# Kernel optimization log

Hardware: AMD Instinct MI355X
Metric: run time of the kernel (lower is better)

Reference implementation:

```python
import jax, jax.numpy as jnp
import numpy as np
from jax import lax

C = 32    # feats_channels
CT = 16   # transform_channels
B, D, H, W = 1, 16, 16, 32  # N = D*H*W = 8192


def _bcast(v):
    return v[None, :, None, None, None]


def conv1(x, w):
    # 1x1x1 Conv3d, no bias: w [O, I], x [b, I, d, h, w]
    return jnp.einsum('oi,bidhw->bodhw', w, x)


def cbr(x, w, s, b):
    # Conv1x1x1 + inference BatchNorm (folded to scale s / bias b) + ReLU
    return jax.nn.relu(conv1(x, w) * _bcast(s) + _bcast(b))


def setup_inputs() -> dict:
    key = jax.random.key(0)
    ks = jax.random.split(key, 16)

    def wmat(k, shape, scale=0.05):
        return jax.random.normal(k, shape, jnp.float32) * scale

    def bn(k, n):
        k1, k2 = jax.random.split(k)
        s = 1.0 + 0.05 * jax.random.normal(k1, (n,), jnp.float32)
        b = 0.05 * jax.random.normal(k2, (n,), jnp.float32)
        return s, b

    inp = {'x': jax.random.normal(ks[0], (B, C, D, H, W), jnp.float32)}
    # query_project: 2 convs (C->CT, CT->CT), each conv+BN+ReLU
    inp['wq1'] = wmat(ks[1], (CT, C));  inp['sq1'], inp['bq1'] = bn(ks[2], CT)
    inp['wq2'] = wmat(ks[3], (CT, CT)); inp['sq2'], inp['bq2'] = bn(ks[4], CT)
    # key_project: 2 convs (2C->CT, CT->CT)
    inp['wk1'] = wmat(ks[5], (CT, 2 * C)); inp['sk1'], inp['bk1'] = bn(ks[6], CT)
    inp['wk2'] = wmat(ks[7], (CT, CT));    inp['sk2'], inp['bk2'] = bn(ks[8], CT)
    # value_project: 1 conv (2C->CT) + BN + ReLU
    inp['wv'] = wmat(ks[9], (CT, 2 * C)); inp['sv'], inp['bv'] = bn(ks[10], CT)
    # out_project: 1 conv (CT->C) + BN + ReLU
    inp['wo'] = wmat(ks[11], (C, CT)); inp['so'], inp['bo'] = bn(ks[12], C)
    # bottleneck: Conv3d(2C->C, k=3, pad=1, no bias) + BN + LeakyReLU(0.1)
    inp['wbot'] = wmat(ks[13], (C, 2 * C, 3, 3, 3), 0.02)
    inp['sbot'], inp['bbot'] = bn(ks[14], C)
    return inp


def reference(x, wq1, sq1, bq1, wq2, sq2, bq2,
              wk1, sk1, bk1, wk2, sk2, bk2,
              wv, sv, bv, wo, so, bo, wbot, sbot, bbot):
    b, c, d, h, w = x.shape
    # AdaptiveAvgPool2d((1,1)) on (b, c*d, h, w) = mean over (h, w) per (c,d);
    # bilinear upsample from 1x1 is a constant broadcast.
    xg = jnp.mean(x, axis=(3, 4), keepdims=True)
    key_feats = jnp.concatenate([jnp.broadcast_to(xg, x.shape), x], axis=1)  # [b, 2c, d, h, w]

    q = cbr(cbr(x, wq1, sq1, bq1), wq2, sq2, bq2)          # [b, CT, d, h, w]
    k = cbr(cbr(key_feats, wk1, sk1, bk1), wk2, sk2, bk2)  # [b, CT, d, h, w]
    v = cbr(key_feats, wv, sv, bv)                          # [b, CT, d, h, w]

    n = d * h * w
    q = q.reshape(b, CT, n).transpose(0, 2, 1)  # [b, N, CT]
    k = k.reshape(b, CT, n)                     # [b, CT, N]
    v = v.reshape(b, CT, n).transpose(0, 2, 1)  # [b, N, CT]

    sim = jnp.einsum('bnc,bcm->bnm', q, k) * (CT ** -0.5)   # [b, N, N]
    sim = jax.nn.softmax(sim, axis=-1)
    ctx = jnp.einsum('bnm,bmc->bnc', sim, v)                # [b, N, CT]
    ctx = ctx.transpose(0, 2, 1).reshape(b, CT, d, h, w)
    ctx = cbr(ctx, wo, so, bo)                              # [b, C, d, h, w]

    fused = jnp.concatenate([x, ctx], axis=1)               # [b, 2C, d, h, w]
    y = lax.conv_general_dilated(
        fused, wbot, window_strides=(1, 1, 1), padding='SAME',
        dimension_numbers=('NCDHW', 'OIDHW', 'NCDHW'))
    y = y * _bcast(sbot) + _bcast(bbot)
    return jnp.where(y > 0, y, 0.1 * y)  # LeakyReLU(0.1)
```

## Files before the change

### kernel.cpp

```cpp
#include <hip/hip_runtime.h>

typedef unsigned int u32;
typedef unsigned short u16;
typedef float f32x16 __attribute__((ext_vector_type(16)));
typedef __bf16 bf16x8 __attribute__((ext_vector_type(8)));
union BF8 { u32 w[4]; bf16x8 v; };

#define DEVI static __device__ __forceinline__
DEVI u32 pk_bf16(float lo, float hi) {
  u32 r;
  asm("v_cvt_pk_bf16_f32 %0, %1, %2" : "=v"(r) : "v"(lo), "v"(hi));
  return r;
}
DEVI u16 bf1(float x) { return (u16)(pk_bf16(x, 0.0f) & 0xffffu); }

#define WB_WREP  0
#define WB_QS    131072
#define WB_K     393216
#define WB_VT    655360
#define WB_FUS   917504

__global__ __launch_bounds__(256) void k_prep(
    const float* __restrict__ x,
    const float* __restrict__ wq1, const float* __restrict__ sq1, const float* __restrict__ bq1,
    const float* __restrict__ wq2, const float* __restrict__ sq2, const float* __restrict__ bq2,
    const float* __restrict__ wk1, const float* __restrict__ sk1, const float* __restrict__ bk1,
    const float* __restrict__ wk2, const float* __restrict__ sk2, const float* __restrict__ bk2,
    const float* __restrict__ wv,  const float* __restrict__ sv,  const float* __restrict__ bv,
    const float* __restrict__ wbot, const float* __restrict__ sbot,
    u16* __restrict__ qs, u16* __restrict__ kbm, u16* __restrict__ vt,
    u16* __restrict__ fus, u16* __restrict__ wrep) {
  const int tid = threadIdx.x;
  const int bid = blockIdx.x;
  if (bid >= 256) {
    const int rb = bid - 256;
#pragma unroll
    for (int e = 0; e < 8; ++e) {
      const int idx = rb * 2048 + tid * 8 + e;
      const int tap = idx >> 11, rem = idx & 2047, o = rem >> 6, i = rem & 63;
      wrep[idx] = bf1(wbot[(o * 64 + i) * 27 + tap] * sbot[o]);
    }
    return;
  }
  __shared__ float H[2][32][17];
  __shared__ float P8[32][8];
  __shared__ float xgs[32];
  const int n0 = bid << 5;
  const int d = n0 >> 9;
  {
    const int c = tid >> 3, part = tid & 7;
    const float4* xp = (const float4*)(x + (c << 13) + (d << 9));
    float s = 0.f;
#pragma unroll
    for (int i = 0; i < 16; ++i) {
      const float4 v4 = xp[part + (i << 3)];
      s += v4.x + v4.y + v4.z + v4.w;
    }
    P8[c][part] = s;
  }
  __syncthreads();
  if (tid < 32) {
    float s = 0.f;
#pragma unroll
    for (int j = 0; j < 8; ++j) s += P8[tid][j];
    xgs[tid] = s * (1.0f / 512.0f);
  }
  __syncthreads();
  const int nl = tid & 31, g = tid >> 5;
  const int n = n0 + nl;
  const int r0 = 2 * g, r1 = r0 + 1;
  float xr[32], xgv[32];
#pragma unroll
  for (int c = 0; c < 32; ++c) xr[c] = x[(c << 13) + n];
#pragma unroll
  for (int c = 0; c < 32; ++c) xgv[c] = xgs[c];

  const float4* wq1f = (const float4*)wq1;
  const float4* wk1f = (const float4*)wk1;
  const float4* wvf  = (const float4*)wv;
  float dq0 = 0.f, dq1 = 0.f, dk0 = 0.f, dk1 = 0.f, dv0 = 0.f, dv1 = 0.f;
#pragma unroll
  for (int c4 = 0; c4 < 8; ++c4) {
    const float4 wa = wq1f[r0 * 8 + c4], wb = wq1f[r1 * 8 + c4];
    dq0 += wa.x * xr[4*c4+0] + wa.y * xr[4*c4+1] + wa.z * xr[4*c4+2] + wa.w * xr[4*c4+3];
    dq1 += wb.x * xr[4*c4+0] + wb.y * xr[4*c4+1] + wb.z * xr[4*c4+2] + wb.w * xr[4*c4+3];
  }
#pragma unroll
  for (int c4 = 0; c4 < 8; ++c4) {
    const float4 ka = wk1f[r0 * 16 + c4], kb = wk1f[r1 * 16 + c4];
    dk0 += ka.x * xgv[4*c4+0] + ka.y * xgv[4*c4+1] + ka.z * xgv[4*c4+2] + ka.w * xgv[4*c4+3];
    dk1 += kb.x * xgv[4*c4+0] + kb.y * xgv[4*c4+1] + kb.z * xgv[4*c4+2] + kb.w * xgv[4*c4+3];
    const float4 va = wvf[r0 * 16 + c4], vb = wvf[r1 * 16 + c4];
    dv0 += va.x * xgv[4*c4+0] + va.y * xgv[4*c4+1] + va.z * xgv[4*c4+2] + va.w * xgv[4*c4+3];
    dv1 += vb.x * xgv[4*c4+0] + vb.y * xgv[4*c4+1] + vb.z * xgv[4*c4+2] + vb.w * xgv[4*c4+3];
  }
#pragma unroll
  for (int c4 = 0; c4 < 8; ++c4) {
    const float4 ka = wk1f[r0 * 16 + 8 + c4], kb = wk1f[r1 * 16 + 8 + c4];
    dk0 += ka.x * xr[4*c4+0] + ka.y * xr[4*c4+1] + ka.z * xr[4*c4+2] + ka.w * xr[4*c4+3];
    dk1 += kb.x * xr[4*c4+0] + kb.y * xr[4*c4+1] + kb.z * xr[4*c4+2] + kb.w * xr[4*c4+3];
    const float4 va = wvf[r0 * 16 + 8 + c4], vb = wvf[r1 * 16 + 8 + c4];
    dv0 += va.x * xr[4*c4+0] + va.y * xr[4*c4+1] + va.z * xr[4*c4+2] + va.w * xr[4*c4+3];
    dv1 += vb.x * xr[4*c4+0] + vb.y * xr[4*c4+1] + vb.z * xr[4*c4+2] + vb.w * xr[4*c4+3];
  }
  const float hq0 = fmaxf(dq0 * sq1[r0] + bq1[r0], 0.f);
  const float hq1 = fmaxf(dq1 * sq1[r1] + bq1[r1], 0.f);
  const float hk0 = fmaxf(dk0 * sk1[r0] + bk1[r0], 0.f);
  const float hk1 = fmaxf(dk1 * sk1[r1] + bk1[r1], 0.f);
  const float hv0 = fmaxf(dv0 * sv[r0] + bv[r0], 0.f);
  const float hv1 = fmaxf(dv1 * sv[r1] + bv[r1], 0.f);
  H[0][nl][r0] = hq0; H[0][nl][r1] = hq1;
  H[1][nl][r0] = hk0; H[1][nl][r1] = hk1;
  vt[(r0 << 13) + n] = bf1(hv0);
  vt[(r1 << 13) + n] = bf1(hv1);
  const int c0 = g << 2;
  *(u32*)(fus + (n << 6) + c0)     = pk_bf16(xr[c0],     xr[c0 + 1]);
  *(u32*)(fus + (n << 6) + c0 + 2) = pk_bf16(xr[c0 + 2], xr[c0 + 3]);
  __syncthreads();

  float eq0 = 0.f, eq1 = 0.f, ek0 = 0.f, ek1 = 0.f;
#pragma unroll
  for (int j = 0; j < 16; ++j) {
    const float hq = H[0][nl][j], hk = H[1][nl][j];
    eq0 += wq2[r0 * 16 + j] * hq;
    eq1 += wq2[r1 * 16 + j] * hq;
    ek0 += wk2[r0 * 16 + j] * hk;
    ek1 += wk2[r1 * 16 + j] * hk;
  }
  const float SC = 0.36067376022224085f;
  const float q0 = fmaxf(eq0 * (sq2[r0] * SC) + bq2[r0] * SC, 0.f);
  const float q1 = fmaxf(eq1 * (sq2[r1] * SC) + bq2[r1] * SC, 0.f);
  const float k0 = fmaxf(ek0 * sk2[r0] + bk2[r0], 0.f);
  const float k1 = fmaxf(ek1 * sk2[r1] + bk2[r1], 0.f);
  *(u32*)(qs  + (n << 4) + r0) = pk_bf16(q0, q1);
  *(u32*)(kbm + (n << 4) + r0) = pk_bf16(k0, k1);
}

__global__ __launch_bounds__(1024) void k_attn(
    const u16* __restrict__ qs, const u16* __restrict__ kbm, const u16* __restrict__ vt,
    const float* __restrict__ wo, const float* __restrict__ so, const float* __restrict__ bo,
    u16* __restrict__ fus) {
  __shared__ float R[16][32][17];
  const int tid = threadIdx.x;
  const int w = tid >> 6, lane = tid & 63;
  const int l31 = lane & 31, h = lane >> 5;
  const int qb = blockIdx.x;

  const bf16x8 qf = *(const bf16x8*)(qs + (((qb << 5) + l31) << 4) + (h << 3));
  f32x16 acc, z;
#pragma unroll
  for (int i = 0; i < 16; ++i) { acc[i] = 0.f; z[i] = 0.f; }

  const u32 fill = (l31 == 16) ? 0x3F803F80u : 0u;
  const int kb0 = w << 9;
  const bool vlane = (l31 < 16);
  const u16* vrow = vt + (l31 << 13) + (h << 3);

  bf16x8 kf_c = *(const bf16x8*)(kbm + ((kb0 + l31) << 4) + (h << 3));
  BF8 V1c, V2c;
#pragma unroll
  for (int j2 = 0; j2 < 4; ++j2) { V1c.w[j2] = fill; V2c.w[j2] = fill; }
  if (vlane) {
    V1c.v = *(const bf16x8*)(vrow + kb0);
    V2c.v = *(const bf16x8*)(vrow + kb0 + 16);
  }

#pragma unroll
  for (int t = 0; t < 16; ++t) {
    const bf16x8 kf = kf_c;
    const BF8 V1 = V1c, V2 = V2c;
    if (t < 15) {
      const int kbn = kb0 + ((t + 1) << 5);
      kf_c = *(const bf16x8*)(kbm + ((kbn + l31) << 4) + (h << 3));
      if (vlane) {
        V1c.v = *(const bf16x8*)(vrow + kbn);
        V2c.v = *(const bf16x8*)(vrow + kbn + 16);
      }
    }
    const f32x16 st = __builtin_amdgcn_mfma_f32_32x32x16_bf16(kf, qf, z, 0, 0, 0);
    float pe[16];
#pragma unroll
    for (int r = 0; r < 16; ++r) pe[r] = __builtin_amdgcn_exp2f(st[r]);
    u32 a0 = pk_bf16(pe[0],  pe[1]),  a1 = pk_bf16(pe[2],  pe[3]);
    u32 a2 = pk_bf16(pe[4],  pe[5]),  a3 = pk_bf16(pe[6],  pe[7]);
    u32 b0 = pk_bf16(pe[8],  pe[9]),  b1 = pk_bf16(pe[10], pe[11]);
    u32 b2 = pk_bf16(pe[12], pe[13]), b3 = pk_bf16(pe[14], pe[15]);
    asm("v_permlane32_swap_b32 %0, %1" : "+v"(a0), "+v"(a2));
    asm("v_permlane32_swap_b32 %0, %1" : "+v"(a1), "+v"(a3));
    asm("v_permlane32_swap_b32 %0, %1" : "+v"(b0), "+v"(b2));
    asm("v_permlane32_swap_b32 %0, %1" : "+v"(b1), "+v"(b3));
    BF8 A1, A2;
    A1.w[0] = a0; A1.w[1] = a1; A1.w[2] = a2; A1.w[3] = a3;
    A2.w[0] = b0; A2.w[1] = b1; A2.w[2] = b2; A2.w[3] = b3;
    acc = __builtin_amdgcn_mfma_f32_32x32x16_bf16(A1.v, V1.v, acc, 0, 0, 0);
    acc = __builtin_amdgcn_mfma_f32_32x32x16_bf16(A2.v, V2.v, acc, 0, 0, 0);
  }
  if (l31 < 17) {
#pragma unroll
    for (int r = 0; r < 16; ++r) {
      const int row = (r & 3) + ((r >> 2) << 3) + (h << 2);
      R[w][row][l31] = acc[r];
    }
  }
  __syncthreads();
  float* Rf = &R[0][0][0];
  if (tid < 544) {
    float s0 = 0.f;
#pragma unroll
    for (int w2 = 0; w2 < 16; ++w2) s0 += Rf[w2 * 544 + tid];
    Rf[tid] = s0;
  }
  __syncthreads();
  if (tid < 512) {
    const int row = tid >> 4;
    const int o0 = (tid & 15) << 1, o1 = o0 + 1;
    const float inv = 1.0f / Rf[row * 17 + 16];
    float d0 = 0.f, d1 = 0.f;
#pragma unroll
    for (int c = 0; c < 16; ++c) {
      const float cv = Rf[row * 17 + c];
      d0 += wo[o0 * 16 + c] * cv;
      d1 += wo[o1 * 16 + c] * cv;
    }
    const float y0 = fmaxf(bo[o0] + so[o0] * d0 * inv, 0.f);
    const float y1 = fmaxf(bo[o1] + so[o1] * d1 * inv, 0.f);
    *(u32*)(fus + (((qb << 5) + row) << 6) + 32 + o0) = pk_bf16(y0, y1);
  }
}

__global__ __launch_bounds__(256) void k_conv(
    const u16* __restrict__ fus, const u16* __restrict__ wrep,
    const float* __restrict__ bbot, float* __restrict__ out) {
  __shared__ float R4[4][1024];
  const int tid = threadIdx.x;
  const int wv = tid >> 6, lane = tid & 63;
  const int l31 = lane & 31, h = lane >> 5;
  const int n0 = blockIdx.x << 5;
  const int dz = n0 >> 9, hy = (n0 >> 5) & 15;
  f32x16 acc0, acc1;
#pragma unroll
  for (int i = 0; i < 16; ++i) { acc0[i] = 0.f; acc1[i] = 0.f; }
  const int tlo = wv * 7;
  const int ntap = (wv == 3) ? 6 : 7;
#pragma unroll
  for (int i = 0; i < 7; ++i) {
    if (i >= ntap) break;
    const int tap = tlo + i;
    const int dd = tap / 9 - 1, dh = (tap / 3) % 3 - 1, dw = tap % 3 - 1;
    if ((unsigned)(dz + dd) >= 16u) continue;
    if ((unsigned)(hy + dh) >= 16u) continue;
    const bool okw = (unsigned)(l31 + dw) < 32u;
    const int nn = n0 + dd * 512 + dh * 32 + dw + l31;
    const u16* wp = wrep + ((tap * 32 + l31) << 6) + (h << 3);
    const u16* bp = fus + (nn << 6) + (h << 3);
#pragma unroll
    for (int c = 0; c < 4; ++c) {
      const bf16x8 af = *(const bf16x8*)(wp + (c << 4));
      BF8 B_;
      B_.w[0] = B_.w[1] = B_.w[2] = B_.w[3] = 0u;
      if (okw) B_.v = *(const bf16x8*)(bp + (c << 4));
      if (i & 1) acc1 = __builtin_amdgcn_mfma_f32_32x32x16_bf16(af, B_.v, acc1, 0, 0, 0);
      else       acc0 = __builtin_amdgcn_mfma_f32_32x32x16_bf16(af, B_.v, acc0, 0, 0, 0);
    }
  }
#pragma unroll
  for (int r = 0; r < 16; ++r) {
    const int row = (r & 3) + ((r >> 2) << 3) + (h << 2);
    R4[wv][(row << 5) + l31] = acc0[r] + acc1[r];
  }
  __syncthreads();
#pragma unroll
  for (int k2 = 0; k2 < 4; ++k2) {
    const int e = tid + (k2 << 8);
    const int row = e >> 5;
    const float yv = R4[0][e] + R4[1][e] + R4[2][e] + R4[3][e] + bbot[row];
    out[(row << 13) + n0 + (e & 31)] = yv > 0.f ? yv : 0.1f * yv;
  }
}

extern "C" void kernel_launch(void* const* d_in, const int* in_sizes, int n_in,
                              void* d_out, int out_size, void* d_ws, size_t ws_size,
                              hipStream_t stream) {
  const float* x    = (const float*)d_in[0];
  const float* wq1  = (const float*)d_in[1];
  const float* sq1  = (const float*)d_in[2];
  const float* bq1  = (const float*)d_in[3];
  const float* wq2  = (const float*)d_in[4];
  const float* sq2  = (const float*)d_in[5];
  const float* bq2  = (const float*)d_in[6];
  const float* wk1  = (const float*)d_in[7];
  const float* sk1  = (const float*)d_in[8];
  const float* bk1  = (const float*)d_in[9];
  const float* wk2  = (const float*)d_in[10];
  const float* sk2  = (const float*)d_in[11];
  const float* bk2  = (const float*)d_in[12];
  const float* wv   = (const float*)d_in[13];
  const float* sv   = (const float*)d_in[14];
  const float* bv   = (const float*)d_in[15];
  const float* wo   = (const float*)d_in[16];
  const float* so   = (const float*)d_in[17];
  const float* bo   = (const float*)d_in[18];
  const float* wbot = (const float*)d_in[19];
  const float* sbot = (const float*)d_in[20];
  const float* bbot = (const float*)d_in[21];
  (void)in_sizes; (void)n_in; (void)out_size; (void)ws_size;

  char* wsb = (char*)d_ws;
  u16* wrep = (u16*)(wsb + WB_WREP);
  u16* qs   = (u16*)(wsb + WB_QS);
  u16* kbm  = (u16*)(wsb + WB_K);
  u16* vt   = (u16*)(wsb + WB_VT);
  u16* fus  = (u16*)(wsb + WB_FUS);
  float* out = (float*)d_out;

  k_prep<<<283, 256, 0, stream>>>(x, wq1, sq1, bq1, wq2, sq2, bq2,
                                  wk1, sk1, bk1, wk2, sk2, bk2,
                                  wv, sv, bv, wbot, sbot,
                                  qs, kbm, vt, fus, wrep);
  k_attn<<<256, 1024, 0, stream>>>(qs, kbm, vt, wo, so, bo, fus);
  k_conv<<<256, 256, 0, stream>>>(fus, wrep, bbot, out);
}
```

Baseline: 36.87 us.

## Split attention accumulators, add MFMA priority, and repartition conv over 8 waves

The attention kernel now uses two independent accumulators for the P·V MFMAs, which breaks the serial dependency chain, and wraps the MFMAs in s_setprio. The conv kernel moves from 4 to 8 waves per block. The 54 half-tap units (27 taps × 2 channel halves) are spread evenly across waves, and fused-input loads are software-prefetched one unit ahead. The aim is more latency hiding and better MFMA issue, at the cost of a larger LDS reduction buffer and more cross-wave partial sums.

Result: faster. 35.90 us (-2.6%).

```diff
diff --git a/kernel.cpp b/kernel.cpp
--- a/kernel.cpp
+++ b/kernel.cpp
@@ -147,9 +147,9 @@
   const int qb = blockIdx.x;
 
   const bf16x8 qf = *(const bf16x8*)(qs + (((qb << 5) + l31) << 4) + (h << 3));
-  f32x16 acc, z;
-#pragma unroll
-  for (int i = 0; i < 16; ++i) { acc[i] = 0.f; z[i] = 0.f; }
+  f32x16 acc_a, acc_b, z;
+#pragma unroll
+  for (int i = 0; i < 16; ++i) { acc_a[i] = 0.f; acc_b[i] = 0.f; z[i] = 0.f; }
 
   const u32 fill = (l31 == 16) ? 0x3F803F80u : 0u;
   const int kb0 = w << 9;
@@ -192,14 +192,16 @@
     BF8 A1, A2;
     A1.w[0] = a0; A1.w[1] = a1; A1.w[2] = a2; A1.w[3] = a3;
     A2.w[0] = b0; A2.w[1] = b1; A2.w[2] = b2; A2.w[3] = b3;
-    acc = __builtin_amdgcn_mfma_f32_32x32x16_bf16(A1.v, V1.v, acc, 0, 0, 0);
-    acc = __builtin_amdgcn_mfma_f32_32x32x16_bf16(A2.v, V2.v, acc, 0, 0, 0);
+    __builtin_amdgcn_s_setprio(1);
+    acc_a = __builtin_amdgcn_mfma_f32_32x32x16_bf16(A1.v, V1.v, acc_a, 0, 0, 0);
+    acc_b = __builtin_amdgcn_mfma_f32_32x32x16_bf16(A2.v, V2.v, acc_b, 0, 0, 0);
+    __builtin_amdgcn_s_setprio(0);
   }
   if (l31 < 17) {
 #pragma unroll
     for (int r = 0; r < 16; ++r) {
       const int row = (r & 3) + ((r >> 2) << 3) + (h << 2);
-      R[w][row][l31] = acc[r];
+      R[w][row][l31] = acc_a[r] + acc_b[r];
     }
   }
   __syncthreads();
@@ -228,10 +230,10 @@
   }
 }
 
-__global__ __launch_bounds__(256) void k_conv(
+__global__ __launch_bounds__(512) void k_conv(
     const u16* __restrict__ fus, const u16* __restrict__ wrep,
     const float* __restrict__ bbot, float* __restrict__ out) {
-  __shared__ float R4[4][1024];
+  __shared__ float R8[8][1024];
   const int tid = threadIdx.x;
   const int wv = tid >> 6, lane = tid & 63;
   const int l31 = lane & 31, h = lane >> 5;
@@ -240,40 +242,59 @@
   f32x16 acc0, acc1;
 #pragma unroll
   for (int i = 0; i < 16; ++i) { acc0[i] = 0.f; acc1[i] = 0.f; }
-  const int tlo = wv * 7;
-  const int ntap = (wv == 3) ? 6 : 7;
-#pragma unroll
-  for (int i = 0; i < 7; ++i) {
-    if (i >= ntap) break;
-    const int tap = tlo + i;
+  const int ulo = (wv * 54) >> 3, uhi = ((wv + 1) * 54) >> 3;
+
+  const u16* bp_c; const u16* wp_c; bool ok_c;
+  {
+    const int tap = ulo >> 1, ch = (ulo & 1) << 1;
     const int dd = tap / 9 - 1, dh = (tap / 3) % 3 - 1, dw = tap % 3 - 1;
-    if ((unsigned)(dz + dd) >= 16u) continue;
-    if ((unsigned)(hy + dh) >= 16u) continue;
-    const bool okw = (unsigned)(l31 + dw) < 32u;
+    ok_c = ((unsigned)(dz + dd) < 16u) & ((unsigned)(hy + dh) < 16u) &
+           ((unsigned)(l31 + dw) < 32u);
     const int nn = n0 + dd * 512 + dh * 32 + dw + l31;
-    const u16* wp = wrep + ((tap * 32 + l31) << 6) + (h << 3);
-    const u16* bp = fus + (nn << 6) + (h << 3);
-#pragma unroll
-    for (int c = 0; c < 4; ++c) {
-      const bf16x8 af = *(const bf16x8*)(wp + (c << 4));
-      BF8 B_;
-      B_.w[0] = B_.w[1] = B_.w[2] = B_.w[3] = 0u;
-      if (okw) B_.v = *(const bf16x8*)(bp + (c << 4));
-      if (i & 1) acc1 = __builtin_amdgcn_mfma_f32_32x32x16_bf16(af, B_.v, acc1, 0, 0, 0);
-      else       acc0 = __builtin_amdgcn_mfma_f32_32x32x16_bf16(af, B_.v, acc0, 0, 0, 0);
-    }
+    bp_c = fus + (nn << 6) + (ch << 4) + (h << 3);
+    wp_c = wrep + ((tap * 32 + l31) << 6) + (ch << 4) + (h << 3);
+  }
+  BF8 B0c, B1c;
+  B0c.w[0] = B0c.w[1] = B0c.w[2] = B0c.w[3] = 0u;
+  B1c.w[0] = B1c.w[1] = B1c.w[2] = B1c.w[3] = 0u;
+  if (ok_c) { B0c.v = *(const bf16x8*)bp_c; B1c.v = *(const bf16x8*)(bp_c + 16); }
+
+  for (int u = ulo; u < uhi; ++u) {
+    const BF8 B0 = B0c, B1 = B1c;
+    const u16* wp = wp_c;
+    if (u + 1 < uhi) {
+      const int un = u + 1;
+      const int tap = un >> 1, ch = (un & 1) << 1;
+      const int dd = tap / 9 - 1, dh = (tap / 3) % 3 - 1, dw = tap % 3 - 1;
+      const bool ok = ((unsigned)(dz + dd) < 16u) & ((unsigned)(hy + dh) < 16u) &
+                      ((unsigned)(l31 + dw) < 32u);
+      const int nn = n0 + dd * 512 + dh * 32 + dw + l31;
+      const u16* bp = fus + (nn << 6) + (ch << 4) + (h << 3);
+      wp_c = wrep + ((tap * 32 + l31) << 6) + (ch << 4) + (h << 3);
+      B0c.w[0] = B0c.w[1] = B0c.w[2] = B0c.w[3] = 0u;
+      B1c.w[0] = B1c.w[1] = B1c.w[2] = B1c.w[3] = 0u;
+      if (ok) { B0c.v = *(const bf16x8*)bp; B1c.v = *(const bf16x8*)(bp + 16); }
+    }
+    const bf16x8 af0 = *(const bf16x8*)wp;
+    const bf16x8 af1 = *(const bf16x8*)(wp + 16);
+    __builtin_amdgcn_s_setprio(1);
+    acc0 = __builtin_amdgcn_mfma_f32_32x32x16_bf16(af0, B0.v, acc0, 0, 0, 0);
+    acc1 = __builtin_amdgcn_mfma_f32_32x32x16_bf16(af1, B1.v, acc1, 0, 0, 0);
+    __builtin_amdgcn_s_setprio(0);
   }
 #pragma unroll
   for (int r = 0; r < 16; ++r) {
     const int row = (r & 3) + ((r >> 2) << 3) + (h << 2);
-    R4[wv][(row << 5) + l31] = acc0[r] + acc1[r];
-  }
-  __syncthreads();
-#pragma unroll
-  for (int k2 = 0; k2 < 4; ++k2) {
-    const int e = tid + (k2 << 8);
+    R8[wv][(row << 5) + l31] = acc0[r] + acc1[r];
+  }
+  __syncthreads();
+#pragma unroll
+  for (int k2 = 0; k2 < 2; ++k2) {
+    const int e = tid + (k2 << 9);
     const int row = e >> 5;
-    const float yv = R4[0][e] + R4[1][e] + R4[2][e] + R4[3][e] + bbot[row];
+    float yv = bbot[row];
+#pragma unroll
+    for (int w2 = 0; w2 < 8; ++w2) yv += R8[w2][e];
     out[(row << 13) + n0 + (e & 31)] = yv > 0.f ? yv : 0.1f * yv;
   }
 }
@@ -318,5 +339,5 @@
                                   wv, sv, bv, wbot, sbot,
                                   qs, kbm, vt, fus, wrep);
   k_attn<<<256, 1024, 0, stream>>>(qs, kbm, vt, wo, so, bo, fus);
-  k_conv<<<256, 256, 0, stream>>>(fus, wrep, bbot, out);
-}
+  k_conv<<<256, 512, 0, stream>>>(fus, wrep, bbot, out);
+}
```
